# Optimization experiments

Measured on AMD Instinct MI355X. Metric: run time of the kernel, lower is better.

Reference implementation:

```python
import jax, jax.numpy as jnp
import numpy as np

NUM_CODES = 128
CODE_DIM = 64
B, D, T = 64, 64, 8192


def setup_inputs() -> dict:
    key = jax.random.key(0)
    k1, k2 = jax.random.split(key)
    z_e = jax.random.normal(k1, (B, D, T), dtype=jnp.float32)
    centroids = jax.random.normal(k2, (NUM_CODES, CODE_DIM), dtype=jnp.float32)
    return {"z_e": z_e, "centroids": centroids}


def reference(z_e, centroids):
    b, d, t = z_e.shape
    K = centroids.shape[0]
    # [B, D, T] -> [B*T, D]
    z = jnp.transpose(z_e, (0, 2, 1)).reshape(b * t, d)
    # squared euclidean distances: ||z||^2 - 2 z C^T + ||C||^2  -> [N, K]
    dists = (
        jnp.sum(z * z, axis=1, keepdims=True)
        - 2.0 * (z @ centroids.T)
        + jnp.sum(centroids * centroids, axis=1)[None, :]
    )
    idx = jnp.argmin(dists, axis=1)  # [N]
    idx_bt = idx.reshape(b, t)[:, None, :]  # [B, 1, T]
    counts = jnp.bincount(idx, length=K).astype(jnp.float32)  # [K]
    p = jnp.maximum(counts / float(idx.size), 1e-12)
    H = -jnp.sum(p * jnp.log(p))
    perp = jnp.exp(H)
    usage = jnp.mean((counts > 0).astype(jnp.float32))
    return idx_bt, perp, usage
```

## Files before the change

kernel.cpp:

```cpp
#include <hip/hip_runtime.h>
#include <math.h>

#define NUM_CODES 128
#define CODE_DIM  64
#define B_ 64
#define D_ 64
#define T_ 8192
#define N_TOK (B_ * T_)

__global__ __launch_bounds__(128) void kmeans_prep(
    const float* __restrict__ centroids, float* __restrict__ c2h,
    unsigned int* __restrict__ counts)
{
    int k = threadIdx.x;
    const float* cp = centroids + k * CODE_DIM;
    float s0 = 0.f, s1 = 0.f, s2 = 0.f, s3 = 0.f;
    #pragma unroll
    for (int d = 0; d < CODE_DIM; d += 4) {
        s0 = fmaf(cp[d + 0], cp[d + 0], s0);
        s1 = fmaf(cp[d + 1], cp[d + 1], s1);
        s2 = fmaf(cp[d + 2], cp[d + 2], s2);
        s3 = fmaf(cp[d + 3], cp[d + 3], s3);
    }
    c2h[k] = 0.5f * ((s0 + s1) + (s2 + s3));
    counts[k] = 0u;
}

__global__ __launch_bounds__(256, 4) void kmeans_assign(
    const float* __restrict__ z_e, const float* __restrict__ centroids,
    const float* __restrict__ c2h, unsigned int* __restrict__ counts,
    float* __restrict__ out_idx)
{
    __shared__ float        cl[NUM_CODES * CODE_DIM];
    __shared__ float        c2l[NUM_CODES];
    __shared__ unsigned int hist[NUM_CODES];

    const int tid = threadIdx.x;

    {
        const float4* src = (const float4*)centroids;
        float4*       dst = (float4*)cl;
        #pragma unroll
        for (int r = 0; r < 8; ++r) dst[r * 256 + tid] = src[r * 256 + tid];
        if (tid < NUM_CODES) { c2l[tid] = c2h[tid]; hist[tid] = 0u; }
    }

    const int n = blockIdx.x * 256 + tid;
    const int b = n >> 13;
    const int t = n & (T_ - 1);
    const float* zp = z_e + (size_t)b * (size_t)(D_ * T_) + t;
    float z[64];
    #pragma unroll
    for (int d = 0; d < 64; ++d) z[d] = zp[(size_t)d * T_];

    __syncthreads();

    float best = -3.4e38f;
    int   bi   = 0;

    #pragma unroll 2
    for (int k = 0; k < NUM_CODES; ++k) {
        const float4* cp4 = (const float4*)(cl + k * CODE_DIM);
        float a0 = -c2l[k], a1 = 0.f;
        #pragma unroll
        for (int q = 0; q < 16; ++q) {
            float4 c = cp4[q];
            a0 = fmaf(c.x, z[4*q + 0], a0);
            a1 = fmaf(c.y, z[4*q + 1], a1);
            a0 = fmaf(c.z, z[4*q + 2], a0);
            a1 = fmaf(c.w, z[4*q + 3], a1);
        }
        float m = a0 + a1;
        if (m > best) { best = m; bi = k; }
    }

    out_idx[n] = (float)bi;

    atomicAdd(&hist[bi], 1u);
    __syncthreads();
    if (tid < NUM_CODES) {
        unsigned int h = hist[tid];
        if (h) atomicAdd(&counts[tid], h);
    }
}

__global__ __launch_bounds__(128) void kmeans_finalize(
    const unsigned int* __restrict__ counts, float* __restrict__ out)
{
    const int k = threadIdx.x;
    unsigned int c = counts[k];
    float p = fmaxf((float)c * (1.0f / (float)N_TOK), 1e-12f);
    float h = -p * logf(p);
    float u = (c > 0u) ? 1.0f : 0.0f;

    __shared__ float sh[NUM_CODES];
    __shared__ float su[NUM_CODES];
    sh[k] = h; su[k] = u;
    __syncthreads();
    for (int s = 64; s > 0; s >>= 1) {
        if (k < s) { sh[k] += sh[k + s]; su[k] += su[k + s]; }
        __syncthreads();
    }
    if (k == 0) {
        out[N_TOK + 0] = expf(sh[0]);
        out[N_TOK + 1] = su[0] * (1.0f / 128.f);
    }
}

extern "C" void kernel_launch(void* const* d_in, const int* in_sizes, int n_in,
                              void* d_out, int out_size, void* d_ws, size_t ws_size,
                              hipStream_t stream)
{
    const float* z_e       = (const float*)d_in[0];
    const float* centroids = (const float*)d_in[1];
    float* out = (float*)d_out;

    float*        c2h    = (float*)d_ws;
    unsigned int* counts = (unsigned int*)d_ws + NUM_CODES;

    kmeans_prep<<<1, 128, 0, stream>>>(centroids, c2h, counts);
    kmeans_assign<<<N_TOK / 256, 256, 0, stream>>>(z_e, centroids, c2h, counts, out);
    kmeans_finalize<<<1, 128, 0, stream>>>(counts, out);
}
```

Before: 302.4 us.

## Split codebook across waves and process two tokens per thread

Each block now handles 128 tokens. Every thread loads two adjacent tokens with float2 loads, and each of the four waves scans only a quarter of the codes, so each centroid LDS read feeds two tokens' FMAs. Per-wave partial argmins go to shared memory and wave 0 merges them, then writes the indices and updates the histogram. The cost is twice the registers for z (launch bounds lowered to 2 blocks per SM), twice as many blocks each reloading the 32KB codebook, and an extra sync plus merge step. Ties merge in ascending wave order with a strict greater-than, which keeps the lowest index first.

Measured after the change: 281.1 us. 1.08x faster.

```diff
diff --git a/kernel.cpp b/kernel.cpp
--- a/kernel.cpp
+++ b/kernel.cpp
@@ -26,16 +26,21 @@
     counts[k] = 0u;
 }
 
-__global__ __launch_bounds__(256, 4) void kmeans_assign(
+__global__ __launch_bounds__(256, 2) void kmeans_assign(
     const float* __restrict__ z_e, const float* __restrict__ centroids,
     const float* __restrict__ c2h, unsigned int* __restrict__ counts,
     float* __restrict__ out_idx)
 {
     __shared__ float        cl[NUM_CODES * CODE_DIM];
     __shared__ float        c2l[NUM_CODES];
+    __shared__ float        sb[4][128];
+    __shared__ int          si[4][128];
     __shared__ unsigned int hist[NUM_CODES];
 
-    const int tid = threadIdx.x;
+    const int tid   = threadIdx.x;
+    const int lane  = tid & 63;
+    const int w     = tid >> 6;
+    const int kbase = w * 32;
 
     {
         const float4* src = (const float4*)centroids;
@@ -45,38 +50,64 @@
         if (tid < NUM_CODES) { c2l[tid] = c2h[tid]; hist[tid] = 0u; }
     }
 
-    const int n = blockIdx.x * 256 + tid;
-    const int b = n >> 13;
-    const int t = n & (T_ - 1);
-    const float* zp = z_e + (size_t)b * (size_t)(D_ * T_) + t;
-    float z[64];
+    const int n0 = blockIdx.x * 128 + 2 * lane;
+    const int b  = n0 >> 13;
+    const int t0 = n0 & (T_ - 1);
+    const float* zp = z_e + (size_t)b * (size_t)(D_ * T_) + t0;
+    float za[64], zb[64];
     #pragma unroll
-    for (int d = 0; d < 64; ++d) z[d] = zp[(size_t)d * T_];
+    for (int d = 0; d < 64; ++d) {
+        float2 v = *(const float2*)(zp + (size_t)d * T_);
+        za[d] = v.x; zb[d] = v.y;
+    }
 
     __syncthreads();
 
-    float best = -3.4e38f;
-    int   bi   = 0;
+    float bA = -3.4e38f, bB = -3.4e38f;
+    int   iA = kbase,    iB = kbase;
 
     #pragma unroll 2
-    for (int k = 0; k < NUM_CODES; ++k) {
+    for (int i = 0; i < 32; ++i) {
+        const int k = kbase + i;
         const float4* cp4 = (const float4*)(cl + k * CODE_DIM);
-        float a0 = -c2l[k], a1 = 0.f;
+        float nh = -c2l[k];
+        float a0 = nh, a1 = 0.f, b0 = nh, b1 = 0.f;
         #pragma unroll
         for (int q = 0; q < 16; ++q) {
             float4 c = cp4[q];
-            a0 = fmaf(c.x, z[4*q + 0], a0);
-            a1 = fmaf(c.y, z[4*q + 1], a1);
-            a0 = fmaf(c.z, z[4*q + 2], a0);
-            a1 = fmaf(c.w, z[4*q + 3], a1);
+            a0 = fmaf(c.x, za[4*q + 0], a0);
+            a1 = fmaf(c.y, za[4*q + 1], a1);
+            a0 = fmaf(c.z, za[4*q + 2], a0);
+            a1 = fmaf(c.w, za[4*q + 3], a1);
+            b0 = fmaf(c.x, zb[4*q + 0], b0);
+            b1 = fmaf(c.y, zb[4*q + 1], b1);
+            b0 = fmaf(c.z, zb[4*q + 2], b0);
+            b1 = fmaf(c.w, zb[4*q + 3], b1);
         }
-        float m = a0 + a1;
-        if (m > best) { best = m; bi = k; }
+        float ma = a0 + a1, mb = b0 + b1;
+        if (ma > bA) { bA = ma; iA = k; }
+        if (mb > bB) { bB = mb; iB = k; }
     }
 
-    out_idx[n] = (float)bi;
+    sb[w][2*lane]   = bA;  si[w][2*lane]   = iA;
+    sb[w][2*lane+1] = bB;  si[w][2*lane+1] = iB;
+    __syncthreads();
 
-    atomicAdd(&hist[bi], 1u);
+    const int nblk = blockIdx.x * 128;
+    if (w == 0) {
+        #pragma unroll
+        for (int r = 0; r < 2; ++r) {
+            int tok = lane + 64 * r;
+            float bb = sb[0][tok]; int bi = si[0][tok];
+            #pragma unroll
+            for (int ww = 1; ww < 4; ++ww) {
+                float v = sb[ww][tok];
+                if (v > bb) { bb = v; bi = si[ww][tok]; }
+            }
+            out_idx[nblk + tok] = (float)bi;
+            atomicAdd(&hist[bi], 1u);
+        }
+    }
     __syncthreads();
     if (tid < NUM_CODES) {
         unsigned int h = hist[tid];
@@ -119,6 +150,6 @@
     unsigned int* counts = (unsigned int*)d_ws + NUM_CODES;
 
     kmeans_prep<<<1, 128, 0, stream>>>(centroids, c2h, counts);
-    kmeans_assign<<<N_TOK / 256, 256, 0, stream>>>(z_e, centroids, c2h, counts, out);
+    kmeans_assign<<<N_TOK / 128, 256, 0, stream>>>(z_e, centroids, c2h, counts, out);
     kmeans_finalize<<<1, 128, 0, stream>>>(counts, out);
 }
```

## Compute distances with split-bf16 MFMA and rescore top-2 candidates in fp32

Applied to the files above, without the earlier changes.

The scalar fp32 distance loop is replaced by bf16 MFMA matrix multiplies. Inputs and centroids are each split into three bf16 pieces so the product approaches fp32 accuracy, and the prep kernel prebuilds the centroid pieces in MFMA fragment layout. Each wave then keeps the top-2 codes per token, and those two are rescored in exact fp32 to guard against argmin ties or errors. This swaps the ALU-bound FMA loop for matrix-core throughput. In exchange it reads z twice, runs the rescoring on only 64 threads per block, and uses smaller 64-token blocks.

After: 344.6 us. +14.0%, slower.

```diff
diff --git a/kernel.cpp b/kernel.cpp
--- a/kernel.cpp
+++ b/kernel.cpp
@@ -8,75 +8,210 @@
 #define T_ 8192
 #define N_TOK (B_ * T_)
 
-__global__ __launch_bounds__(128) void kmeans_prep(
-    const float* __restrict__ centroids, float* __restrict__ c2h,
-    unsigned int* __restrict__ counts)
-{
-    int k = threadIdx.x;
-    const float* cp = centroids + k * CODE_DIM;
-    float s0 = 0.f, s1 = 0.f, s2 = 0.f, s3 = 0.f;
-    #pragma unroll
-    for (int d = 0; d < CODE_DIM; d += 4) {
-        s0 = fmaf(cp[d + 0], cp[d + 0], s0);
-        s1 = fmaf(cp[d + 1], cp[d + 1], s1);
-        s2 = fmaf(cp[d + 2], cp[d + 2], s2);
-        s3 = fmaf(cp[d + 3], cp[d + 3], s3);
-    }
-    c2h[k] = 0.5f * ((s0 + s1) + (s2 + s3));
-    counts[k] = 0u;
-}
-
-__global__ __launch_bounds__(256, 4) void kmeans_assign(
+typedef __attribute__((ext_vector_type(8))) short bf16x8;
+typedef __attribute__((ext_vector_type(4))) float f32x4;
+
+union BU { uint4 q; bf16x8 v; unsigned short h[8]; unsigned int u[4]; };
+
+__device__ __forceinline__ unsigned short bf16_rne(float x) {
+    unsigned int u = __float_as_uint(x);
+    unsigned int r = u + 0x7fffu + ((u >> 16) & 1u);
+    return (unsigned short)(r >> 16);
+}
+__device__ __forceinline__ float bf16_f(unsigned short h) {
+    return __uint_as_float(((unsigned int)h) << 16);
+}
+
+__global__ __launch_bounds__(256) void kmeans_prep(
+    const float* __restrict__ centroids, float* __restrict__ ws_f)
+{
+    const int tid = threadIdx.x;
+    float*        c2h    = ws_f;
+    unsigned int* counts = (unsigned int*)(ws_f + 128);
+    unsigned int* frag   = (unsigned int*)(ws_f + 256);
+
+    if (tid < NUM_CODES) {
+        const float* cp = centroids + tid * CODE_DIM;
+        float s0 = 0.f, s1 = 0.f, s2 = 0.f, s3 = 0.f;
+        #pragma unroll
+        for (int d = 0; d < CODE_DIM; d += 4) {
+            s0 = fmaf(cp[d + 0], cp[d + 0], s0);
+            s1 = fmaf(cp[d + 1], cp[d + 1], s1);
+            s2 = fmaf(cp[d + 2], cp[d + 2], s2);
+            s3 = fmaf(cp[d + 3], cp[d + 3], s3);
+        }
+        c2h[tid] = 0.5f * ((s0 + s1) + (s2 + s3));
+        counts[tid] = 0u;
+    }
+
+    for (int e = tid; e < 3072; e += 256) {
+        int fid  = e >> 6;
+        int lane = e & 63;
+        int ks   = fid & 1;
+        int nt   = (fid >> 1) & 7;
+        int p    = fid >> 4;
+        int code = nt * 16 + (lane & 15);
+        int k0   = ks * 32 + (lane >> 4) * 8;
+        const float* cp = centroids + code * CODE_DIM + k0;
+        unsigned short hb[8];
+        #pragma unroll
+        for (int j = 0; j < 8; ++j) {
+            float x = cp[j];
+            unsigned short b1 = bf16_rne(x);
+            float r1 = x - bf16_f(b1);
+            unsigned short b2 = bf16_rne(r1);
+            float r2 = r1 - bf16_f(b2);
+            unsigned short b3 = bf16_rne(r2);
+            hb[j] = (p == 0) ? b1 : (p == 1) ? b2 : b3;
+        }
+        unsigned int* dst = frag + fid * 256 + lane * 4;
+        #pragma unroll
+        for (int w2 = 0; w2 < 4; ++w2)
+            dst[w2] = (unsigned int)hb[2 * w2] | ((unsigned int)hb[2 * w2 + 1] << 16);
+    }
+}
+
+__global__ __launch_bounds__(256, 3) void kmeans_assign(
     const float* __restrict__ z_e, const float* __restrict__ centroids,
-    const float* __restrict__ c2h, unsigned int* __restrict__ counts,
+    const float* __restrict__ ws_f, unsigned int* __restrict__ counts,
     float* __restrict__ out_idx)
 {
-    __shared__ float        cl[NUM_CODES * CODE_DIM];
+    __shared__ unsigned int bfr[12288];
     __shared__ float        c2l[NUM_CODES];
+    __shared__ unsigned int cand[64];
     __shared__ unsigned int hist[NUM_CODES];
 
-    const int tid = threadIdx.x;
+    const int tid  = threadIdx.x;
+    const int lane = tid & 63;
+    const int w    = tid >> 6;
 
     {
-        const float4* src = (const float4*)centroids;
-        float4*       dst = (float4*)cl;
-        #pragma unroll
-        for (int r = 0; r < 8; ++r) dst[r * 256 + tid] = src[r * 256 + tid];
-        if (tid < NUM_CODES) { c2l[tid] = c2h[tid]; hist[tid] = 0u; }
-    }
-
-    const int n = blockIdx.x * 256 + tid;
-    const int b = n >> 13;
-    const int t = n & (T_ - 1);
-    const float* zp = z_e + (size_t)b * (size_t)(D_ * T_) + t;
-    float z[64];
-    #pragma unroll
-    for (int d = 0; d < 64; ++d) z[d] = zp[(size_t)d * T_];
-
-    __syncthreads();
-
-    float best = -3.4e38f;
-    int   bi   = 0;
-
-    #pragma unroll 2
-    for (int k = 0; k < NUM_CODES; ++k) {
-        const float4* cp4 = (const float4*)(cl + k * CODE_DIM);
-        float a0 = -c2l[k], a1 = 0.f;
-        #pragma unroll
-        for (int q = 0; q < 16; ++q) {
-            float4 c = cp4[q];
-            a0 = fmaf(c.x, z[4*q + 0], a0);
-            a1 = fmaf(c.y, z[4*q + 1], a1);
-            a0 = fmaf(c.z, z[4*q + 2], a0);
-            a1 = fmaf(c.w, z[4*q + 3], a1);
-        }
-        float m = a0 + a1;
-        if (m > best) { best = m; bi = k; }
-    }
-
-    out_idx[n] = (float)bi;
-
-    atomicAdd(&hist[bi], 1u);
+        const uint4* src = (const uint4*)(ws_f + 256);
+        uint4*       dst = (uint4*)bfr;
+        #pragma unroll
+        for (int r = 0; r < 12; ++r) dst[r * 256 + tid] = src[r * 256 + tid];
+        if (tid < NUM_CODES) { c2l[tid] = ws_f[tid]; hist[tid] = 0u; }
+    }
+
+    const int base = blockIdx.x * 64;
+    const int b    = base >> 13;
+    const int t0   = base & (T_ - 1);
+    const float* zw = z_e + (size_t)b * (size_t)(D_ * T_) + t0 + w * 16 + (lane & 15);
+
+    BU A1[2], A2[2], A3[2];
+    #pragma unroll
+    for (int ks = 0; ks < 2; ++ks) {
+        const int k0 = ks * 32 + (lane >> 4) * 8;
+        #pragma unroll
+        for (int j = 0; j < 8; ++j) {
+            float x = zw[(size_t)(k0 + j) * T_];
+            unsigned short b1 = bf16_rne(x);
+            float r1 = x - bf16_f(b1);
+            unsigned short b2 = bf16_rne(r1);
+            float r2 = r1 - bf16_f(b2);
+            unsigned short b3 = bf16_rne(r2);
+            A1[ks].h[j] = b1; A2[ks].h[j] = b2; A3[ks].h[j] = b3;
+        }
+    }
+
+    __syncthreads();
+
+    f32x4 acc[8];
+    #pragma unroll
+    for (int nt = 0; nt < 8; ++nt) acc[nt] = (f32x4){0.f, 0.f, 0.f, 0.f};
+
+    const int lbase = lane * 4;
+    #pragma unroll
+    for (int nt = 0; nt < 8; ++nt) {
+        #pragma unroll
+        for (int ks = 0; ks < 2; ++ks) {
+            BU B1, B2, B3;
+            B1.q = *(const uint4*)(bfr + ((0 * 8 + nt) * 2 + ks) * 256 + lbase);
+            B2.q = *(const uint4*)(bfr + ((1 * 8 + nt) * 2 + ks) * 256 + lbase);
+            B3.q = *(const uint4*)(bfr + ((2 * 8 + nt) * 2 + ks) * 256 + lbase);
+            acc[nt] = __builtin_amdgcn_mfma_f32_16x16x32_bf16(A1[ks].v, B1.v, acc[nt], 0, 0, 0);
+            acc[nt] = __builtin_amdgcn_mfma_f32_16x16x32_bf16(A1[ks].v, B2.v, acc[nt], 0, 0, 0);
+            acc[nt] = __builtin_amdgcn_mfma_f32_16x16x32_bf16(A2[ks].v, B1.v, acc[nt], 0, 0, 0);
+            acc[nt] = __builtin_amdgcn_mfma_f32_16x16x32_bf16(A2[ks].v, B2.v, acc[nt], 0, 0, 0);
+            acc[nt] = __builtin_amdgcn_mfma_f32_16x16x32_bf16(A1[ks].v, B3.v, acc[nt], 0, 0, 0);
+            acc[nt] = __builtin_amdgcn_mfma_f32_16x16x32_bf16(A3[ks].v, B1.v, acc[nt], 0, 0, 0);
+        }
+    }
+
+    float s1[4], s2[4]; int c1[4], c2v[4];
+    #pragma unroll
+    for (int j = 0; j < 4; ++j) { s1[j] = s2[j] = -3.4e38f; c1[j] = c2v[j] = 0; }
+    #pragma unroll
+    for (int nt = 0; nt < 8; ++nt) {
+        const int  code = nt * 16 + (lane & 15);
+        const float csub = c2l[code];
+        #pragma unroll
+        for (int j = 0; j < 4; ++j) {
+            float s = acc[nt][j] - csub;
+            if (s > s1[j])      { s2[j] = s1[j]; c2v[j] = c1[j]; s1[j] = s; c1[j] = code; }
+            else if (s > s2[j]) { s2[j] = s;     c2v[j] = code; }
+        }
+    }
+    #pragma unroll
+    for (int m = 1; m <= 8; m <<= 1) {
+        #pragma unroll
+        for (int j = 0; j < 4; ++j) {
+            float os1 = __shfl_xor(s1[j], m); int oc1 = __shfl_xor(c1[j], m);
+            float os2 = __shfl_xor(s2[j], m); int oc2 = __shfl_xor(c2v[j], m);
+            bool a  = (os1 > s1[j]) || (os1 == s1[j] && oc1 < c1[j]);
+            float n1 = a ? os1 : s1[j]; int nc1 = a ? oc1 : c1[j];
+            float l1 = a ? s1[j] : os1; int lc1 = a ? c1[j] : oc1;
+            bool bs = (os2 > s2[j]) || (os2 == s2[j] && oc2 < c2v[j]);
+            float w2 = bs ? os2 : s2[j]; int wc2 = bs ? oc2 : c2v[j];
+            bool c3 = (l1 > w2) || (l1 == w2 && lc1 < wc2);
+            s1[j] = n1; c1[j] = nc1;
+            s2[j] = c3 ? l1 : w2; c2v[j] = c3 ? lc1 : wc2;
+        }
+    }
+    if ((lane & 15) == 0) {
+        const int g = lane >> 4;
+        #pragma unroll
+        for (int j = 0; j < 4; ++j) {
+            int ka = c1[j], kb = c2v[j];
+            int kmin = min(ka, kb), kmax = max(ka, kb);
+            cand[w * 16 + g * 4 + j] = ((unsigned int)kmin << 8) | (unsigned int)kmax;
+        }
+    }
+    __syncthreads();
+
+    if (tid < 64) {
+        unsigned int cp_ = cand[tid];
+        int k1 = (int)(cp_ >> 8), k2 = (int)(cp_ & 255u);
+        const float* zp = z_e + (size_t)b * (size_t)(D_ * T_) + t0 + tid;
+        float z[64];
+        #pragma unroll
+        for (int d = 0; d < 64; ++d) z[d] = zp[(size_t)d * T_];
+
+        float m1, m2;
+        {
+            const float* cp = centroids + k1 * CODE_DIM;
+            float a0 = -c2l[k1], a1 = 0.f;
+            #pragma unroll
+            for (int d = 0; d < 64; d += 2) {
+                a0 = fmaf(cp[d],     z[d],     a0);
+                a1 = fmaf(cp[d + 1], z[d + 1], a1);
+            }
+            m1 = a0 + a1;
+        }
+        {
+            const float* cp = centroids + k2 * CODE_DIM;
+            float a0 = -c2l[k2], a1 = 0.f;
+            #pragma unroll
+            for (int d = 0; d < 64; d += 2) {
+                a0 = fmaf(cp[d],     z[d],     a0);
+                a1 = fmaf(cp[d + 1], z[d + 1], a1);
+            }
+            m2 = a0 + a1;
+        }
+        int bi = (m2 > m1) ? k2 : k1;
+        out_idx[base + tid] = (float)bi;
+        atomicAdd(&hist[bi], 1u);
+    }
     __syncthreads();
     if (tid < NUM_CODES) {
         unsigned int h = hist[tid];
@@ -113,12 +248,11 @@
 {
     const float* z_e       = (const float*)d_in[0];
     const float* centroids = (const float*)d_in[1];
-    float* out = (float*)d_out;
-
-    float*        c2h    = (float*)d_ws;
-    unsigned int* counts = (unsigned int*)d_ws + NUM_CODES;
-
-    kmeans_prep<<<1, 128, 0, stream>>>(centroids, c2h, counts);
-    kmeans_assign<<<N_TOK / 256, 256, 0, stream>>>(z_e, centroids, c2h, counts, out);
+    float* out  = (float*)d_out;
+    float* ws_f = (float*)d_ws;
+    unsigned int* counts = (unsigned int*)(ws_f + 128);
+
+    kmeans_prep<<<1, 256, 0, stream>>>(centroids, ws_f);
+    kmeans_assign<<<N_TOK / 64, 256, 0, stream>>>(z_e, centroids, ws_f, counts, out);
     kmeans_finalize<<<1, 128, 0, stream>>>(counts, out);
 }
```
